# Kernel tuning notes

Measured on AMD Instinct MI355X. Metric: run time of the kernel, lower is better.

## Reference

```python
import jax, jax.numpy as jnp
import numpy as np


def setup_inputs() -> dict:
    key = jax.random.key(0)
    kx, ky = jax.random.split(key)
    n, m, d = 2048, 2048, 16  # d == n_wires
    x = jax.random.normal(kx, (n, d), dtype=jnp.float32)
    y = jax.random.normal(ky, (m, d), dtype=jnp.float32)
    return {"x": x, "y": y}


def reference(x, y):
    # RY gates on distinct wires commute; RY(-y_k) RY(x_k) = RY(x_k - y_k).
    # State = tensor product over wires of RY(x_k - y_k)|0>, so the |0...0>
    # amplitude is prod_k cos((x_k - y_k)/2). Original code stores abs(amplitude).
    half_diff = 0.5 * (x[:, None, :] - y[None, :, :])  # [n, m, d]
    kernel = jnp.abs(jnp.prod(jnp.cos(half_diff), axis=-1))  # [n, m]
    return kernel
```

## Files before the change

kernel.cpp:

```cpp
#include <hip/hip_runtime.h>
#include <hip/hip_bf16.h>


constexpr int D = 16;
constexpr int RSTR = 72;

typedef short  bf16x8 __attribute__((ext_vector_type(8)));
typedef float  f32x16 __attribute__((ext_vector_type(16)));

static __device__ inline unsigned int pk2(float a, float b) {
    __hip_bfloat16 ha = __float2bfloat16(a);
    __hip_bfloat16 hb = __float2bfloat16(b);
    unsigned short ua, ub;
    __builtin_memcpy(&ua, &ha, 2);
    __builtin_memcpy(&ub, &hb, 2);
    return (unsigned int)ua | ((unsigned int)ub << 16);
}

__global__ __launch_bounds__(256)
void qkern(const float* __restrict__ x, const float* __restrict__ y,
           float* __restrict__ out, int m) {
    __shared__ unsigned short Al[64 * RSTR];
    __shared__ unsigned short Bl[64 * RSTR];

    const int tid   = threadIdx.x;
    const int row0b = blockIdx.x * 64;
    const int col0b = blockIdx.y * 64;

    {
        const int u    = tid >> 1;
        const int half = tid & 1;
        const bool isrow = (u < 64);
        const float* src = isrow ? (x + (size_t)(row0b + u) * D)
                                 : (y + (size_t)(col0b + (u - 64)) * D);
        unsigned short* dst = (isrow ? Al + (size_t)u * RSTR
                                     : Bl + (size_t)(u - 64) * RSTR);
        const float scale = isrow ? 0.5f : 1.0f;

        float f[4][4];
#pragma unroll
        for (int pp = 0; pp < 4; ++pp) {
            const int p = half * 4 + pp;
            const float a0 = src[2 * p], a1 = src[2 * p + 1];
            float sm, cm, sp, cp;
            __sincosf(0.5f * (a0 - a1), &sm, &cm);
            __sincosf(0.5f * (a0 + a1), &sp, &cp);
            f[pp][0] = scale * cm; f[pp][1] = scale * sm;
            f[pp][2] = scale * cp; f[pp][3] = scale * sp;
        }
#pragma unroll
        for (int qq = 0; qq < 2; ++qq) {
            const int q = half * 2 + qq;
            const float* fa = f[2 * qq];
            const float* fb = f[2 * qq + 1];
            uint4 lo, hi;
            lo.x = pk2(fa[0] * fb[0], fa[0] * fb[1]);
            lo.y = pk2(fa[0] * fb[2], fa[0] * fb[3]);
            lo.z = pk2(fa[1] * fb[0], fa[1] * fb[1]);
            lo.w = pk2(fa[1] * fb[2], fa[1] * fb[3]);
            hi.x = pk2(fa[2] * fb[0], fa[2] * fb[1]);
            hi.y = pk2(fa[2] * fb[2], fa[2] * fb[3]);
            hi.z = pk2(fa[3] * fb[0], fa[3] * fb[1]);
            hi.w = pk2(fa[3] * fb[2], fa[3] * fb[3]);
            *(uint4*)(dst + q * 16)     = lo;
            *(uint4*)(dst + q * 16 + 8) = hi;
        }
    }
    __syncthreads();

    const int wave = tid >> 6;
    const int lane = tid & 63;
    const int l31  = lane & 31;
    const int kh   = lane >> 5;
    const int rw   = (wave >> 1) * 32;
    const int cw   = (wave & 1) * 32;

    const f32x16 zc = {0.f};

    f32x16 prod;
    {
        const bf16x8 a0 = *(const bf16x8*)(Al + (size_t)(rw + l31) * RSTR + 0 * 16 + kh * 8);
        const bf16x8 b0 = *(const bf16x8*)(Bl + (size_t)(cw + l31) * RSTR + 0 * 16 + kh * 8);
        prod = __builtin_amdgcn_mfma_f32_32x32x16_bf16(a0, b0, zc, 0, 0, 0);
    }
#pragma unroll
    for (int q = 1; q < 4; ++q) {
        const bf16x8 aq = *(const bf16x8*)(Al + (size_t)(rw + l31) * RSTR + q * 16 + kh * 8);
        const bf16x8 bq = *(const bf16x8*)(Bl + (size_t)(cw + l31) * RSTR + q * 16 + kh * 8);
        const f32x16 acc = __builtin_amdgcn_mfma_f32_32x32x16_bf16(aq, bq, zc, 0, 0, 0);
        prod *= acc;
    }

    const int ocol = col0b + cw + l31;
    float* base = out + (size_t)(row0b + rw + 4 * kh) * m + ocol;
#pragma unroll
    for (int r = 0; r < 16; ++r) {
        const int row_off = (r & 3) + 8 * (r >> 2);
        __builtin_nontemporal_store(fabsf(prod[r]), base + (size_t)row_off * m);
    }
}

extern "C" void kernel_launch(void* const* d_in, const int* in_sizes, int n_in,
                              void* d_out, int out_size, void* d_ws, size_t ws_size,
                              hipStream_t stream) {
    const float* x = (const float*)d_in[0];
    const float* y = (const float*)d_in[1];
    float* out = (float*)d_out;
    const int n = in_sizes[0] / D;
    const int m = in_sizes[1] / D;

    dim3 grid(n / 64, m / 64);
    qkern<<<grid, 256, 0, stream>>>(x, y, out, m);
}
```

Baseline: 60.73 us.

## Enlarge block tile to 128x128 with each wave computing four column subtiles

Each block now covers a 128x128 output tile instead of 64x64. Each wave keeps its A fragments in registers and loops over four 32-column subtiles. This halves the redundant per-row sincos/outer-product preprocessing and LDS fill per output element. The cost is a 4x smaller grid (256 blocks), which lowers occupancy and latency hiding for a store-bound kernel.

```diff
diff --git a/kernel.cpp b/kernel.cpp
--- a/kernel.cpp
+++ b/kernel.cpp
@@ -20,39 +20,36 @@
 __global__ __launch_bounds__(256)
 void qkern(const float* __restrict__ x, const float* __restrict__ y,
            float* __restrict__ out, int m) {
-    __shared__ unsigned short Al[64 * RSTR];
-    __shared__ unsigned short Bl[64 * RSTR];
+    __shared__ unsigned short Al[128 * RSTR];
+    __shared__ unsigned short Bl[128 * RSTR];
 
     const int tid   = threadIdx.x;
-    const int row0b = blockIdx.x * 64;
-    const int col0b = blockIdx.y * 64;
+    const int row0b = blockIdx.x * 128;
+    const int col0b = blockIdx.y * 128;
 
     {
-        const int u    = tid >> 1;
-        const int half = tid & 1;
-        const bool isrow = (u < 64);
+        const int u = tid;
+        const bool isrow = (u < 128);
         const float* src = isrow ? (x + (size_t)(row0b + u) * D)
-                                 : (y + (size_t)(col0b + (u - 64)) * D);
-        unsigned short* dst = (isrow ? Al + (size_t)u * RSTR
-                                     : Bl + (size_t)(u - 64) * RSTR);
+                                 : (y + (size_t)(col0b + (u - 128)) * D);
+        unsigned short* dst = isrow ? (Al + (size_t)u * RSTR)
+                                    : (Bl + (size_t)(u - 128) * RSTR);
         const float scale = isrow ? 0.5f : 1.0f;
 
-        float f[4][4];
+        float f[8][4];
 #pragma unroll
-        for (int pp = 0; pp < 4; ++pp) {
-            const int p = half * 4 + pp;
+        for (int p = 0; p < 8; ++p) {
             const float a0 = src[2 * p], a1 = src[2 * p + 1];
             float sm, cm, sp, cp;
             __sincosf(0.5f * (a0 - a1), &sm, &cm);
             __sincosf(0.5f * (a0 + a1), &sp, &cp);
-            f[pp][0] = scale * cm; f[pp][1] = scale * sm;
-            f[pp][2] = scale * cp; f[pp][3] = scale * sp;
+            f[p][0] = scale * cm; f[p][1] = scale * sm;
+            f[p][2] = scale * cp; f[p][3] = scale * sp;
         }
 #pragma unroll
-        for (int qq = 0; qq < 2; ++qq) {
-            const int q = half * 2 + qq;
-            const float* fa = f[2 * qq];
-            const float* fb = f[2 * qq + 1];
+        for (int q = 0; q < 4; ++q) {
+            const float* fa = f[2 * q];
+            const float* fb = f[2 * q + 1];
             uint4 lo, hi;
             lo.x = pk2(fa[0] * fb[0], fa[0] * fb[1]);
             lo.y = pk2(fa[0] * fb[2], fa[0] * fb[3]);
@@ -72,31 +69,36 @@
     const int lane = tid & 63;
     const int l31  = lane & 31;
     const int kh   = lane >> 5;
-    const int rw   = (wave >> 1) * 32;
-    const int cw   = (wave & 1) * 32;
+    const int rw   = wave * 32;
 
     const f32x16 zc = {0.f};
 
-    f32x16 prod;
-    {
-        const bf16x8 a0 = *(const bf16x8*)(Al + (size_t)(rw + l31) * RSTR + 0 * 16 + kh * 8);
-        const bf16x8 b0 = *(const bf16x8*)(Bl + (size_t)(cw + l31) * RSTR + 0 * 16 + kh * 8);
-        prod = __builtin_amdgcn_mfma_f32_32x32x16_bf16(a0, b0, zc, 0, 0, 0);
-    }
+    bf16x8 af[4];
 #pragma unroll
-    for (int q = 1; q < 4; ++q) {
-        const bf16x8 aq = *(const bf16x8*)(Al + (size_t)(rw + l31) * RSTR + q * 16 + kh * 8);
-        const bf16x8 bq = *(const bf16x8*)(Bl + (size_t)(cw + l31) * RSTR + q * 16 + kh * 8);
-        const f32x16 acc = __builtin_amdgcn_mfma_f32_32x32x16_bf16(aq, bq, zc, 0, 0, 0);
-        prod *= acc;
-    }
+    for (int q = 0; q < 4; ++q)
+        af[q] = *(const bf16x8*)(Al + (size_t)(rw + l31) * RSTR + q * 16 + kh * 8);
 
-    const int ocol = col0b + cw + l31;
-    float* base = out + (size_t)(row0b + rw + 4 * kh) * m + ocol;
 #pragma unroll
-    for (int r = 0; r < 16; ++r) {
-        const int row_off = (r & 3) + 8 * (r >> 2);
-        __builtin_nontemporal_store(fabsf(prod[r]), base + (size_t)row_off * m);
+    for (int cb = 0; cb < 4; ++cb) {
+        const int cw = cb * 32;
+        f32x16 prod;
+        {
+            const bf16x8 b0 = *(const bf16x8*)(Bl + (size_t)(cw + l31) * RSTR + kh * 8);
+            prod = __builtin_amdgcn_mfma_f32_32x32x16_bf16(af[0], b0, zc, 0, 0, 0);
+        }
+#pragma unroll
+        for (int q = 1; q < 4; ++q) {
+            const bf16x8 bq = *(const bf16x8*)(Bl + (size_t)(cw + l31) * RSTR + q * 16 + kh * 8);
+            const f32x16 acc = __builtin_amdgcn_mfma_f32_32x32x16_bf16(af[q], bq, zc, 0, 0, 0);
+            prod *= acc;
+        }
+
+        float* base = out + (size_t)(row0b + rw + 4 * kh) * m + col0b + cw + l31;
+#pragma unroll
+        for (int r = 0; r < 16; ++r) {
+            const int row_off = (r & 3) + 8 * (r >> 2);
+            __builtin_nontemporal_store(fabsf(prod[r]), base + (size_t)row_off * m);
+        }
     }
 }
 
@@ -109,6 +111,6 @@
     const int n = in_sizes[0] / D;
     const int m = in_sizes[1] / D;
 
-    dim3 grid(n / 64, m / 64);
+    dim3 grid(n / 128, m / 128);
     qkern<<<grid, 256, 0, stream>>>(x, y, out, m);
 }
```

Result: no change. 61.16 us (+0.7%).
